# Kernel tuning notes

Measured on AMD Instinct MI355X. Metric: run time of the kernel, lower is better.

## Reference

```python
import jax, jax.numpy as jnp
import numpy as np

B, K, D = 128, 32, 1024
E = 32
H = int(D * 0.25)  # d_hidden = d_block * moe_ratio


def _rsqrt_uniform(key, shape, d):
    bound = d ** -0.5
    return jax.random.uniform(key, shape, jnp.float32, -bound, bound)


def setup_inputs() -> dict:
    key = jax.random.key(0)
    ks = jax.random.split(key, 7)
    return {
        "x": jax.random.normal(ks[0], (B, K, D), jnp.float32),
        "router_w": _rsqrt_uniform(ks[1], (E, D), D),   # nn.Linear(d_block, num_experts).weight
        "router_b": _rsqrt_uniform(ks[2], (E,), D),
        "weights1": _rsqrt_uniform(ks[3], (E, D, H), H),
        "bias1": _rsqrt_uniform(ks[4], (E, H), H),
        "weights2": _rsqrt_uniform(ks[5], (E, H, D), D),
        "bias2": _rsqrt_uniform(ks[6], (E, D), D),
    }


def reference(x, router_w, router_b, weights1, bias1, weights2, bias2):
    b, k, d = x.shape
    x_flat = x.reshape(-1, d)                      # [N, D], N = B*K
    n = x_flat.shape[0]
    # top-1 router (argmax of logits, like torch.argmax)
    logits = x_flat @ router_w.T + router_b        # [N, E]
    routed_idx = jnp.argmax(logits, axis=-1)       # [N]

    # Each expert is a 2-layer MLP; note the original applies act1 (ReLU)
    # after BOTH layers, and dropout=0.0 is an identity.
    def expert_mlp(w1, b1, w2, b2):
        h = jax.nn.relu(x_flat @ w1 + b1)          # [N, H]
        return jax.nn.relu(h @ w2 + b2)            # [N, D]

    y_all = jax.vmap(expert_mlp)(weights1, bias1, weights2, bias2)  # [E, N, D]
    out_flat = y_all[routed_idx, jnp.arange(n)]    # select routed expert per token
    return out_flat.reshape(b, k, d)
```

## Files before the change

kernel.cpp:

```cpp
#include <hip/hip_runtime.h>


#define N_TOK 4096
#define DDIM  1024
#define HDIM  256
#define NEXP  32
#define TPX   136

typedef __attribute__((ext_vector_type(8))) short bf16x8;
typedef __attribute__((ext_vector_type(4))) float f32x4;

__device__ __forceinline__ unsigned short f2bf(float f) {
  union { float f; unsigned u; } v; v.f = f;
  unsigned r = v.u + 0x7FFFu + ((v.u >> 16) & 1u);
  return (unsigned short)(r >> 16);
}
__device__ __forceinline__ float bf2f(unsigned short h) {
  union { unsigned u; float f; } v; v.u = ((unsigned)h) << 16;
  return v.f;
}
__device__ __forceinline__ int swz(int row, int kk) {
  return row * 72 + (kk ^ (((row >> 3) & 7) << 3));
}

__global__ __launch_bounds__(512) void router_kernel(
    const float* __restrict__ x, const float* __restrict__ rw,
    const float* __restrict__ rb, int* __restrict__ routed) {
  __shared__ float red[8][64][8];
  int b = blockIdx.x;
  int t = threadIdx.x, w = t >> 6, l = t & 63;
  int m = l & 15, kb = l >> 4;
  int tok = b * 16 + m;
  int kbase = w * 128;
  bf16x8 wh[2][4], wl[2][4];
#pragma unroll
  for (int h = 0; h < 2; h++) {
    const float* wp = rw + (size_t)(m + h * 16) * DDIM + kbase + kb * 8;
#pragma unroll
    for (int q = 0; q < 4; q++) {
      float4 f0 = *(const float4*)(wp + q * 32);
      float4 f1 = *(const float4*)(wp + q * 32 + 4);
      float fv[8] = {f0.x, f0.y, f0.z, f0.w, f1.x, f1.y, f1.z, f1.w};
      bf16x8 hi, lo;
#pragma unroll
      for (int i = 0; i < 8; i++) {
        unsigned short hh = f2bf(fv[i]);
        hi[i] = (short)hh;
        lo[i] = (short)f2bf(fv[i] - bf2f(hh));
      }
      wh[h][q] = hi; wl[h][q] = lo;
    }
  }
  const float* xrow = x + (size_t)tok * DDIM + kbase + kb * 8;
  f32x4 acc0 = {0.f,0.f,0.f,0.f}, acc1 = {0.f,0.f,0.f,0.f};
#pragma unroll
  for (int q = 0; q < 4; q++) {
    float4 xa = *(const float4*)(xrow + q * 32);
    float4 xc = *(const float4*)(xrow + q * 32 + 4);
    float xv[8] = {xa.x, xa.y, xa.z, xa.w, xc.x, xc.y, xc.z, xc.w};
    bf16x8 xhi, xlo;
#pragma unroll
    for (int i = 0; i < 8; i++) {
      unsigned short hh = f2bf(xv[i]);
      xhi[i] = (short)hh;
      xlo[i] = (short)f2bf(xv[i] - bf2f(hh));
    }
    acc0 = __builtin_amdgcn_mfma_f32_16x16x32_bf16(xhi, wh[0][q], acc0, 0, 0, 0);
    acc0 = __builtin_amdgcn_mfma_f32_16x16x32_bf16(xlo, wh[0][q], acc0, 0, 0, 0);
    acc0 = __builtin_amdgcn_mfma_f32_16x16x32_bf16(xhi, wl[0][q], acc0, 0, 0, 0);
    acc0 = __builtin_amdgcn_mfma_f32_16x16x32_bf16(xlo, wl[0][q], acc0, 0, 0, 0);
    acc1 = __builtin_amdgcn_mfma_f32_16x16x32_bf16(xhi, wh[1][q], acc1, 0, 0, 0);
    acc1 = __builtin_amdgcn_mfma_f32_16x16x32_bf16(xlo, wh[1][q], acc1, 0, 0, 0);
    acc1 = __builtin_amdgcn_mfma_f32_16x16x32_bf16(xhi, wl[1][q], acc1, 0, 0, 0);
    acc1 = __builtin_amdgcn_mfma_f32_16x16x32_bf16(xlo, wl[1][q], acc1, 0, 0, 0);
  }
  *(f32x4*)&red[w][l][0] = acc0;
  *(f32x4*)&red[w][l][4] = acc1;
  __syncthreads();
  if (w == 0) {
    f32x4 s0 = {0.f,0.f,0.f,0.f}, s1 = {0.f,0.f,0.f,0.f};
#pragma unroll
    for (int ww = 0; ww < 8; ww++) {
      s0 += *(const f32x4*)&red[ww][l][0];
      s1 += *(const f32x4*)&red[ww][l][4];
    }
    float rb0 = rb[m], rb1 = rb[16 + m];
#pragma unroll
    for (int r = 0; r < 4; r++) {
      float v0 = s0[r] + rb0;
      float v1 = s1[r] + rb1;
      float val = v0; int idx = m;
      if (v1 > v0) { val = v1; idx = 16 + m; }
#pragma unroll
      for (int s = 1; s < 16; s <<= 1) {
        float ov = __shfl_xor(val, s);
        int oi = __shfl_xor(idx, s);
        if (ov > val || (ov == val && oi < idx)) { val = ov; idx = oi; }
      }
      if (m == 0) routed[b * 16 + kb * 4 + r] = idx;
    }
  }
}

__global__ __launch_bounds__(512) void scan_scatter_kernel(const int* __restrict__ routed,
    int* __restrict__ meta, int* __restrict__ order) {
  __shared__ int scnt[NEXP];
  __shared__ int scur[NEXP];
  int t = threadIdx.x;
  if (t < NEXP) scnt[t] = 0;
  __syncthreads();
  for (int n = t; n < N_TOK; n += 512) atomicAdd(&scnt[routed[n]], 1);
  __syncthreads();
  if (t < NEXP) {
    int c = scnt[t];
    int nt = (c + 31) >> 5;
    int ic = c;
#pragma unroll
    for (int s = 1; s < NEXP; s <<= 1) {
      int pc = __shfl_up(ic, s);
      if (t >= s) ic += pc;
    }
    int off = ic - c;
    scur[t] = off;
    int cls = t & 7, pos = t >> 3;
    int rank = 0;
#pragma unroll
    for (int j = 0; j < 4; j++) {
      int v = __shfl(nt, cls + j * 8);
      if (pos > j) rank += v;
    }
    for (int s2 = 0; s2 < nt; s2++) {
      int nr = c - s2 * 32; if (nr > 32) nr = 32;
      meta[8 + cls + 8 * (rank + s2)] = (t << 24) | (nr << 16) | (off + s2 * 32);
    }
    if (pos == 3) meta[cls] = rank + nt;
  }
  __syncthreads();
  for (int n = t; n < N_TOK; n += 512) {
    int e = routed[n];
    int p = atomicAdd(&scur[e], 1);
    order[p] = n;
  }
}

template <int KDIM, int NTOT, bool A_FP32, bool OUT_BF16>
__global__ __launch_bounds__(512) void expert_gemm_kernel(
    const void* __restrict__ a_src, const float* __restrict__ wsrc,
    const float* __restrict__ bias, const int* __restrict__ meta,
    const int* __restrict__ order, void* __restrict__ outp) {
  constexpr int NCH = KDIM / 64;
  constexpr int NSLAB = NTOT / 128;
  __shared__ unsigned short AT[2][32 * 72];
  __shared__ unsigned short BT[2][128 * 72];
  int bid = blockIdx.x, xcd = bid & 7, r = bid >> 3;
  int ntc = meta[xcd];
  if (r >= ntc * NSLAB) return;
  int y = r / ntc, rank = r - y * ntc;
  int info = meta[8 + xcd + 8 * rank];
  int e = info >> 24, nrow = (info >> 16) & 0xff, ts = info & 0xffff;
  int c0 = y * 128;
  int t = threadIdx.x, w = t >> 6, l = t & 63, m = l & 15, kb = l >> 4;
  int atr = t >> 4, ak4 = (t & 15) * 4;
  int bcn = t & 127, bkg = t >> 7;
  int atok = order[ts + (atr < nrow ? atr : nrow - 1)];
  const float* aF = (const float*)a_src + (size_t)atok * KDIM + ak4;
  const unsigned short* aH = (const unsigned short*)a_src + (size_t)atok * KDIM + ak4;
  const float* bS = wsrc + (size_t)e * KDIM * NTOT + (size_t)(bkg * 16) * NTOT + c0 + bcn;

  float4 nAf[2]; ushort4 nAh[2];
  float nB[2][16];
  auto LOADC = [&](int c, int rb) {
    if constexpr (A_FP32) nAf[rb] = *(const float4*)(aF + c * 64);
    else                  nAh[rb] = *(const ushort4*)(aH + c * 64);
#pragma unroll
    for (int j = 0; j < 16; j++)
      nB[rb][j] = bS[(size_t)(c * 64 + j) * NTOT];
  };

  f32x4 acc0 = {0.f,0.f,0.f,0.f}, acc1 = {0.f,0.f,0.f,0.f};
  LOADC(0, 0);
  LOADC(1, 1);
#pragma unroll
  for (int c = 0; c < NCH; c++) {
    const int p = c & 1;
    ushort4 av;
    if constexpr (A_FP32) {
      av.x = f2bf(nAf[p].x); av.y = f2bf(nAf[p].y);
      av.z = f2bf(nAf[p].z); av.w = f2bf(nAf[p].w);
    } else av = nAh[p];
    *(ushort4*)&AT[p][swz(atr, ak4)] = av;
#pragma unroll
    for (int j = 0; j < 4; j++) {
      ushort4 pv;
      pv.x = f2bf(nB[p][4*j]);   pv.y = f2bf(nB[p][4*j+1]);
      pv.z = f2bf(nB[p][4*j+2]); pv.w = f2bf(nB[p][4*j+3]);
      *(ushort4*)&BT[p][swz(bcn, bkg * 16 + 4 * j)] = pv;
    }
    if (c + 2 < NCH) LOADC(c + 2, p);
    asm volatile("s_waitcnt lgkmcnt(0)" ::: "memory");
    __builtin_amdgcn_s_barrier();
#pragma unroll
    for (int ks = 0; ks < 2; ks++) {
      int kk = ks * 32 + kb * 8;
      bf16x8 bfr = *(const bf16x8*)&BT[p][swz(w * 16 + m, kk)];
      bf16x8 a0  = *(const bf16x8*)&AT[p][swz(m, kk)];
      bf16x8 a1  = *(const bf16x8*)&AT[p][swz(16 + m, kk)];
      acc0 = __builtin_amdgcn_mfma_f32_16x16x32_bf16(a0, bfr, acc0, 0, 0, 0);
      acc1 = __builtin_amdgcn_mfma_f32_16x16x32_bf16(a1, bfr, acc1, 0, 0, 0);
    }
  }
  int col = c0 + w * 16 + m;
  float bz = bias[e * NTOT + col];
#pragma unroll
  for (int r2 = 0; r2 < 4; r2++) {
    int r0 = kb * 4 + r2;
    if (r0 < nrow) {
      int tok = order[ts + r0];
      float v = acc0[r2] + bz; v = v > 0.f ? v : 0.f;
      if constexpr (OUT_BF16)
        ((unsigned short*)outp)[(size_t)tok * NTOT + col] = f2bf(v);
      else
        ((float*)outp)[(size_t)tok * NTOT + col] = v;
    }
    int r1 = 16 + kb * 4 + r2;
    if (r1 < nrow) {
      int tok = order[ts + r1];
      float v = acc1[r2] + bz; v = v > 0.f ? v : 0.f;
      if constexpr (OUT_BF16)
        ((unsigned short*)outp)[(size_t)tok * NTOT + col] = f2bf(v);
      else
        ((float*)outp)[(size_t)tok * NTOT + col] = v;
    }
  }
}


extern "C" void kernel_launch(void* const* d_in, const int* in_sizes, int n_in,
                              void* d_out, int out_size, void* d_ws, size_t ws_size,
                              hipStream_t stream) {
  const float* x  = (const float*)d_in[0];
  const float* rw = (const float*)d_in[1];
  const float* rb = (const float*)d_in[2];
  const float* w1 = (const float*)d_in[3];
  const float* b1 = (const float*)d_in[4];
  const float* w2 = (const float*)d_in[5];
  const float* b2 = (const float*)d_in[6];
  float* out = (float*)d_out;

  char* ws = (char*)d_ws;
  unsigned short* hb = (unsigned short*)(ws + 0);
  int* routed = (int*)(ws + 2097152);
  int* order  = (int*)(ws + 2113536);
  int* meta   = (int*)(ws + 2129920);

  router_kernel<<<dim3(256), dim3(512), 0, stream>>>(x, rw, rb, routed);
  scan_scatter_kernel<<<dim3(1), dim3(512), 0, stream>>>(routed, meta, order);
  expert_gemm_kernel<DDIM, HDIM, true, true>
      <<<dim3(8 * TPX * (HDIM / 128)), dim3(512), 0, stream>>>(
      x, w1, b1, meta, order, hb);
  expert_gemm_kernel<HDIM, DDIM, false, false>
      <<<dim3(8 * TPX * (DDIM / 128)), dim3(512), 0, stream>>>(
      hb, w2, b2, meta, order, out);
}
```

Measured before the change: 54.52 us.

## Fuse router with scan and run both expert GEMMs in one persistent kernel

The scan/scatter step now runs in the last router block, chosen through an atomic completion counter, so one kernel launch goes away. The two expert GEMM launches become a single persistent kernel of 256 blocks. Each block first does its layer-1 tiles and bumps a per-expert counter, then does its layer-2 tiles after spinning until that expert's hidden rows are complete. This cuts launch gaps and lets layer 2 overlap layer 1 across experts. In exchange it adds a memset, spin-wait synchronisation whose progress depends on co-residency of the persistent blocks, and fewer blocks than the old grids had.

```diff
diff --git a/kernel.cpp b/kernel.cpp
--- a/kernel.cpp
+++ b/kernel.cpp
@@ -23,10 +23,14 @@
   return row * 72 + (kk ^ (((row >> 3) & 7) << 3));
 }
 
-__global__ __launch_bounds__(512) void router_kernel(
+__global__ __launch_bounds__(512) void router_scan_kernel(
     const float* __restrict__ x, const float* __restrict__ rw,
-    const float* __restrict__ rb, int* __restrict__ routed) {
+    const float* __restrict__ rb, int* __restrict__ routed,
+    int* __restrict__ meta, int* __restrict__ order, int* __restrict__ done) {
   __shared__ float red[8][64][8];
+  __shared__ int scnt[NEXP];
+  __shared__ int scur[NEXP];
+  __shared__ int lastflag;
   int b = blockIdx.x;
   int t = threadIdx.x, w = t >> 6, l = t & 63;
   int m = l & 15, kb = l >> 4;
@@ -100,13 +104,15 @@
       if (m == 0) routed[b * 16 + kb * 4 + r] = idx;
     }
   }
-}
-
-__global__ __launch_bounds__(512) void scan_scatter_kernel(const int* __restrict__ routed,
-    int* __restrict__ meta, int* __restrict__ order) {
-  __shared__ int scnt[NEXP];
-  __shared__ int scur[NEXP];
-  int t = threadIdx.x;
+  __syncthreads();
+  if (t == 0) {
+    __threadfence();
+    int v = atomicAdd(done, 1);
+    lastflag = (v == 255);
+    if (lastflag) __threadfence();
+  }
+  __syncthreads();
+  if (!lastflag) return;
   if (t < NEXP) scnt[t] = 0;
   __syncthreads();
   for (int n = t; n < N_TOK; n += 512) atomicAdd(&scnt[routed[n]], 1);
@@ -114,6 +120,7 @@
   if (t < NEXP) {
     int c = scnt[t];
     int nt = (c + 31) >> 5;
+    meta[1096 + t] = nt;
     int ic = c;
 #pragma unroll
     for (int s = 1; s < NEXP; s <<= 1) {
@@ -144,21 +151,12 @@
 }
 
 template <int KDIM, int NTOT, bool A_FP32, bool OUT_BF16>
-__global__ __launch_bounds__(512) void expert_gemm_kernel(
+__device__ __forceinline__ void gemm_tile(
     const void* __restrict__ a_src, const float* __restrict__ wsrc,
-    const float* __restrict__ bias, const int* __restrict__ meta,
-    const int* __restrict__ order, void* __restrict__ outp) {
+    const float* __restrict__ bias, const int* __restrict__ order,
+    void* __restrict__ outp, int e, int nrow, int ts, int c0,
+    unsigned short AT[2][32 * 72], unsigned short BT[2][128 * 72]) {
   constexpr int NCH = KDIM / 64;
-  constexpr int NSLAB = NTOT / 128;
-  __shared__ unsigned short AT[2][32 * 72];
-  __shared__ unsigned short BT[2][128 * 72];
-  int bid = blockIdx.x, xcd = bid & 7, r = bid >> 3;
-  int ntc = meta[xcd];
-  if (r >= ntc * NSLAB) return;
-  int y = r / ntc, rank = r - y * ntc;
-  int info = meta[8 + xcd + 8 * rank];
-  int e = info >> 24, nrow = (info >> 16) & 0xff, ts = info & 0xffff;
-  int c0 = y * 128;
   int t = threadIdx.x, w = t >> 6, l = t & 63, m = l & 15, kb = l >> 4;
   int atr = t >> 4, ak4 = (t & 15) * 4;
   int bcn = t & 127, bkg = t >> 7;
@@ -169,12 +167,12 @@
 
   float4 nAf[2]; ushort4 nAh[2];
   float nB[2][16];
-  auto LOADC = [&](int c, int rb) {
-    if constexpr (A_FP32) nAf[rb] = *(const float4*)(aF + c * 64);
-    else                  nAh[rb] = *(const ushort4*)(aH + c * 64);
+  auto LOADC = [&](int c, int rbuf) {
+    if constexpr (A_FP32) nAf[rbuf] = *(const float4*)(aF + c * 64);
+    else                  nAh[rbuf] = *(const ushort4*)(aH + c * 64);
 #pragma unroll
     for (int j = 0; j < 16; j++)
-      nB[rb][j] = bS[(size_t)(c * 64 + j) * NTOT];
+      nB[rbuf][j] = bS[(size_t)(c * 64 + j) * NTOT];
   };
 
   f32x4 acc0 = {0.f,0.f,0.f,0.f}, acc1 = {0.f,0.f,0.f,0.f};
@@ -231,6 +229,42 @@
       else
         ((float*)outp)[(size_t)tok * NTOT + col] = v;
     }
+  }
+}
+
+__global__ __launch_bounds__(512, 2) void moe_persist_kernel(
+    const float* __restrict__ x, const float* __restrict__ w1,
+    const float* __restrict__ b1, const float* __restrict__ w2,
+    const float* __restrict__ b2, unsigned short* __restrict__ hb,
+    float* __restrict__ out, const int* __restrict__ meta,
+    const int* __restrict__ order, int* __restrict__ l1done) {
+  __shared__ unsigned short AT[2][32 * 72];
+  __shared__ unsigned short BT[2][128 * 72];
+  int bid = blockIdx.x, xcd = bid & 7, r = bid >> 3;
+  int ntc = meta[xcd];
+  int t = threadIdx.x;
+  for (int s = r; s < ntc * 2; s += 32) {
+    int y = (s < ntc) ? 0 : 1, rank = (s < ntc) ? s : s - ntc;
+    int info = meta[8 + xcd + 8 * rank];
+    int e = info >> 24, nrow = (info >> 16) & 0xff, ts = info & 0xffff;
+    gemm_tile<DDIM, HDIM, true, true>(x, w1, b1, order, hb, e, nrow, ts, y * 128, AT, BT);
+    __syncthreads();
+    if (t == 0)
+      __hip_atomic_fetch_add(&l1done[e], 1, __ATOMIC_RELEASE, __HIP_MEMORY_SCOPE_AGENT);
+  }
+  for (int s = r; s < ntc * 8; s += 32) {
+    int y = s / ntc, rank = s - y * ntc;
+    int info = meta[8 + xcd + 8 * rank];
+    int e = info >> 24, nrow = (info >> 16) & 0xff, ts = info & 0xffff;
+    if (t == 0) {
+      int need = 2 * meta[1096 + e];
+      while (__hip_atomic_load(&l1done[e], __ATOMIC_RELAXED, __HIP_MEMORY_SCOPE_AGENT) < need)
+        __builtin_amdgcn_s_sleep(8);
+      (void)__hip_atomic_load(&l1done[e], __ATOMIC_ACQUIRE, __HIP_MEMORY_SCOPE_AGENT);
+    }
+    __syncthreads();
+    gemm_tile<HDIM, DDIM, false, false>(hb, w2, b2, order, out, e, nrow, ts, y * 128, AT, BT);
+    __syncthreads();
   }
 }
 
@@ -252,13 +286,12 @@
   int* routed = (int*)(ws + 2097152);
   int* order  = (int*)(ws + 2113536);
   int* meta   = (int*)(ws + 2129920);
-
-  router_kernel<<<dim3(256), dim3(512), 0, stream>>>(x, rw, rb, routed);
-  scan_scatter_kernel<<<dim3(1), dim3(512), 0, stream>>>(routed, meta, order);
-  expert_gemm_kernel<DDIM, HDIM, true, true>
-      <<<dim3(8 * TPX * (HDIM / 128)), dim3(512), 0, stream>>>(
-      x, w1, b1, meta, order, hb);
-  expert_gemm_kernel<HDIM, DDIM, false, false>
-      <<<dim3(8 * TPX * (DDIM / 128)), dim3(512), 0, stream>>>(
-      hb, w2, b2, meta, order, out);
-}
+  int* done   = (int*)(ws + 2134528);
+  int* l1done = (int*)(ws + 2134532);
+
+  hipMemsetAsync(done, 0, 4 + 128, stream);
+  router_scan_kernel<<<dim3(256), dim3(512), 0, stream>>>(
+      x, rw, rb, routed, meta, order, done);
+  moe_persist_kernel<<<dim3(256), dim3(512), 0, stream>>>(
+      x, w1, b1, w2, b2, hb, out, meta, order, l1done);
+}
```

Measured after the change: 97.17 us. 1.78x slower.

## Fuse router and scan via last-block atomic; widen B-tile LDS stores to 16 bytes

Applied to the files above, without the earlier changes.

Merges the routing kernel and the single-block scan/scatter kernel into one launch. A global atomic counter marks the last block to finish, and that block does the expert counting and scatter. A memset of the counter is added to the stream. It also changes the weight-tile staging so each thread converts and writes 8 consecutive bf16 values as one 16-byte LDS store instead of four 8-byte stores, which changes the k-row assignment per thread.

```diff
diff --git a/kernel.cpp b/kernel.cpp
--- a/kernel.cpp
+++ b/kernel.cpp
@@ -23,10 +23,14 @@
   return row * 72 + (kk ^ (((row >> 3) & 7) << 3));
 }
 
-__global__ __launch_bounds__(512) void router_kernel(
+__global__ __launch_bounds__(512) void router_scan_kernel(
     const float* __restrict__ x, const float* __restrict__ rw,
-    const float* __restrict__ rb, int* __restrict__ routed) {
+    const float* __restrict__ rb, int* __restrict__ routed,
+    int* __restrict__ meta, int* __restrict__ order, int* __restrict__ done) {
   __shared__ float red[8][64][8];
+  __shared__ int scnt[NEXP];
+  __shared__ int scur[NEXP];
+  __shared__ int lastflag;
   int b = blockIdx.x;
   int t = threadIdx.x, w = t >> 6, l = t & 63;
   int m = l & 15, kb = l >> 4;
@@ -100,13 +104,15 @@
       if (m == 0) routed[b * 16 + kb * 4 + r] = idx;
     }
   }
-}
-
-__global__ __launch_bounds__(512) void scan_scatter_kernel(const int* __restrict__ routed,
-    int* __restrict__ meta, int* __restrict__ order) {
-  __shared__ int scnt[NEXP];
-  __shared__ int scur[NEXP];
-  int t = threadIdx.x;
+  __syncthreads();
+  if (t == 0) {
+    __threadfence();
+    int v = atomicAdd(done, 1);
+    lastflag = (v == 255);
+    if (lastflag) __threadfence();
+  }
+  __syncthreads();
+  if (!lastflag) return;
   if (t < NEXP) scnt[t] = 0;
   __syncthreads();
   for (int n = t; n < N_TOK; n += 512) atomicAdd(&scnt[routed[n]], 1);
@@ -165,16 +171,18 @@
   int atok = order[ts + (atr < nrow ? atr : nrow - 1)];
   const float* aF = (const float*)a_src + (size_t)atok * KDIM + ak4;
   const unsigned short* aH = (const unsigned short*)a_src + (size_t)atok * KDIM + ak4;
-  const float* bS = wsrc + (size_t)e * KDIM * NTOT + (size_t)(bkg * 16) * NTOT + c0 + bcn;
+  const float* bS = wsrc + (size_t)e * KDIM * NTOT + c0 + bcn;
 
   float4 nAf[2]; ushort4 nAh[2];
-  float nB[2][16];
-  auto LOADC = [&](int c, int rb) {
-    if constexpr (A_FP32) nAf[rb] = *(const float4*)(aF + c * 64);
-    else                  nAh[rb] = *(const ushort4*)(aH + c * 64);
-#pragma unroll
-    for (int j = 0; j < 16; j++)
-      nB[rb][j] = bS[(size_t)(c * 64 + j) * NTOT];
+  float nB[2][2][8];
+  auto LOADC = [&](int c, int rbuf) {
+    if constexpr (A_FP32) nAf[rbuf] = *(const float4*)(aF + c * 64);
+    else                  nAh[rbuf] = *(const ushort4*)(aH + c * 64);
+#pragma unroll
+    for (int u = 0; u < 2; u++)
+#pragma unroll
+      for (int j = 0; j < 8; j++)
+        nB[rbuf][u][j] = bS[(size_t)(c * 64 + (bkg + 4 * u) * 8 + j) * NTOT];
   };
 
   f32x4 acc0 = {0.f,0.f,0.f,0.f}, acc1 = {0.f,0.f,0.f,0.f};
@@ -190,11 +198,11 @@
     } else av = nAh[p];
     *(ushort4*)&AT[p][swz(atr, ak4)] = av;
 #pragma unroll
-    for (int j = 0; j < 4; j++) {
-      ushort4 pv;
-      pv.x = f2bf(nB[p][4*j]);   pv.y = f2bf(nB[p][4*j+1]);
-      pv.z = f2bf(nB[p][4*j+2]); pv.w = f2bf(nB[p][4*j+3]);
-      *(ushort4*)&BT[p][swz(bcn, bkg * 16 + 4 * j)] = pv;
+    for (int u = 0; u < 2; u++) {
+      bf16x8 pv;
+#pragma unroll
+      for (int j = 0; j < 8; j++) pv[j] = (short)f2bf(nB[p][u][j]);
+      *(bf16x8*)&BT[p][swz(bcn, (bkg + 4 * u) * 8)] = pv;
     }
     if (c + 2 < NCH) LOADC(c + 2, p);
     asm volatile("s_waitcnt lgkmcnt(0)" ::: "memory");
@@ -252,9 +260,11 @@
   int* routed = (int*)(ws + 2097152);
   int* order  = (int*)(ws + 2113536);
   int* meta   = (int*)(ws + 2129920);
-
-  router_kernel<<<dim3(256), dim3(512), 0, stream>>>(x, rw, rb, routed);
-  scan_scatter_kernel<<<dim3(1), dim3(512), 0, stream>>>(routed, meta, order);
+  int* done   = (int*)(ws + 2134528);
+
+  hipMemsetAsync(done, 0, 4, stream);
+  router_scan_kernel<<<dim3(256), dim3(512), 0, stream>>>(
+      x, rw, rb, routed, meta, order, done);
   expert_gemm_kernel<DDIM, HDIM, true, true>
       <<<dim3(8 * TPX * (HDIM / 128)), dim3(512), 0, stream>>>(
       x, w1, b1, meta, order, hb);
```

Measured after the change: 63.66 us. +16.8%, slower.
